# Performance work log

Measured on AMD Instinct MI355X. Metric: run time of the kernel, lower is better.

## Reference

```python
import jax, jax.numpy as jnp
import numpy as np
from jax import lax

C = 256; A = 3; FH = 160; FW = 160
IMG_H = 640.0; IMG_W = 640.0; STRIDE = 4.0; ANCHOR_SIZE = 64.0
OBJ_THR = 0.5; IOU_THR = 0.7; PRE_NMS = 2000; TOP_K = 1000
BN_EPS = 1e-5; NEG = -1e9


def setup_inputs() -> dict:
    key = jax.random.key(0)
    ks = jax.random.split(key, 4)
    s = 0.02
    return {
        "x": jax.random.normal(ks[0], (1, C, FH, FW), jnp.float32),
        "conv_w": jax.random.normal(ks[1], (C, C, 3, 3), jnp.float32) * s,
        "conv_b": jnp.zeros((C,), jnp.float32),
        "bn_gamma": jnp.ones((C,), jnp.float32),
        "bn_beta": jnp.zeros((C,), jnp.float32),
        "bn_mean": jnp.zeros((C,), jnp.float32),
        "bn_var": jnp.ones((C,), jnp.float32),
        "det_w": jax.random.normal(ks[2], (A, C), jnp.float32) * s,
        "det_b": jnp.zeros((A,), jnp.float32),
        "reg_w": jax.random.normal(ks[3], (4 * A, C), jnp.float32) * s,
        "reg_b": jnp.zeros((4 * A,), jnp.float32),
    }


def _make_anchors():
    ars = jnp.array([0.5, 1.0, 2.0], jnp.float32)
    h = ANCHOR_SIZE * jnp.sqrt(ars)
    w = ANCHOR_SIZE / jnp.sqrt(ars)
    base = jnp.stack([-w / 2, -h / 2, w / 2, h / 2], axis=1)  # (A,4)
    sx = jnp.arange(FW, dtype=jnp.float32) * STRIDE
    sy = jnp.arange(FH, dtype=jnp.float32) * STRIDE
    yy, xx = jnp.meshgrid(sy, sx, indexing='ij')  # (FH,FW)
    shifts = jnp.stack([xx, yy, xx, yy], axis=-1)  # (FH,FW,4)
    anchors = base[:, None, None, :] + shifts[None]  # (A,FH,FW,4), anchor-major like RPNHead formatting
    return anchors.reshape(-1, 4)


def _clip(boxes):
    return jnp.stack([
        jnp.clip(boxes[:, 0], 0.0, IMG_W),
        jnp.clip(boxes[:, 1], 0.0, IMG_H),
        jnp.clip(boxes[:, 2], 0.0, IMG_W),
        jnp.clip(boxes[:, 3], 0.0, IMG_H),
    ], axis=1)


def _apply_deltas(boxes, deltas):
    w = boxes[:, 2] - boxes[:, 0]
    h = boxes[:, 3] - boxes[:, 1]
    cx = boxes[:, 0] + 0.5 * w
    cy = boxes[:, 1] + 0.5 * h
    pcx = deltas[:, 0] * w + cx
    pcy = deltas[:, 1] * h + cy
    pw = w * jnp.exp(deltas[:, 2])
    ph = h * jnp.exp(deltas[:, 3])
    return jnp.stack([pcx - 0.5 * pw, pcy - 0.5 * ph, pcx + 0.5 * pw, pcy + 0.5 * ph], axis=1)


def _iou_matrix(b):
    area = (b[:, 2] - b[:, 0]) * (b[:, 3] - b[:, 1])
    lt = jnp.maximum(b[:, None, :2], b[None, :, :2])
    rb = jnp.minimum(b[:, None, 2:], b[None, :, 2:])
    wh = jnp.clip(rb - lt, 0.0)
    inter = wh[..., 0] * wh[..., 1]
    return inter / (area[:, None] + area[None, :] - inter + 1e-9)


def _forward(x, conv_w, conv_b, bn_gamma, bn_beta, bn_mean, bn_var, det_w, det_b, reg_w, reg_b):
    # shared conv + BN(eval) + ReLU
    y = lax.conv_general_dilated(x, conv_w, (1, 1), 'SAME',
                                 dimension_numbers=('NCHW', 'OIHW', 'NCHW')) + conv_b[None, :, None, None]
    scale = bn_gamma / jnp.sqrt(bn_var + BN_EPS)
    y = (y - bn_mean[None, :, None, None]) * scale[None, :, None, None] + bn_beta[None, :, None, None]
    y = jax.nn.relu(y)
    # 1x1 RPN heads
    logits = jnp.einsum('nchw,oc->nohw', y, det_w) + det_b[None, :, None, None]  # (1,A,FH,FW)
    reg = jnp.einsum('nchw,oc->nohw', y, reg_w) + reg_b[None, :, None, None]     # (1,4A,FH,FW)
    # format per RPNHead: (N,1,A,H,W)->permute->(N,A*H*W) and (N,4,A,H,W)->(N,A*H*W,4)
    obj = logits.reshape(1, 1, A, FH, FW).transpose(0, 2, 3, 4, 1).reshape(-1)   # (A*FH*FW,)
    deltas = reg.reshape(1, 4, A, FH, FW).transpose(0, 2, 3, 4, 1).reshape(-1, 4)
    anchors = _clip(_make_anchors())
    proposals = _apply_deltas(anchors, lax.stop_gradient(deltas))
    # _filter_proposals (batch=1)
    lg = lax.stop_gradient(obj)
    props = _clip(proposals)
    score = jax.nn.sigmoid(lg)
    masked = jnp.where(score > OBJ_THR, lg, NEG)  # threshold mask (step 2)
    top_scores, idx = lax.top_k(masked, PRE_NMS)  # pre-NMS top-k (step 3)
    top_boxes = props[idx]
    valid = top_scores > NEG / 2
    iou = _iou_matrix(top_boxes)
    arange = jnp.arange(PRE_NMS)

    def body(i, keep):
        sup = (iou[i] > IOU_THR) & (arange > i)
        return jnp.where(keep[i], keep & ~sup, keep)

    keep = lax.fori_loop(0, PRE_NMS, body, valid)  # greedy NMS (boxes pre-sorted by score)
    rank = jnp.cumsum(keep) - 1
    sel = keep & (rank < TOP_K)
    slot = jnp.where(sel, rank, TOP_K)  # overflow bucket at TOP_K
    filt_logits = jnp.full((TOP_K + 1,), NEG, jnp.float32).at[slot].set(top_scores)[:TOP_K]
    filt_boxes = jnp.zeros((TOP_K + 1, 4), jnp.float32).at[slot].set(top_boxes)[:TOP_K]
    return (anchors, obj, deltas, filt_logits, filt_boxes)


def reference(x, conv_w, conv_b, bn_gamma, bn_beta, bn_mean, bn_var, det_w, det_b, reg_w, reg_b):
    return _forward(x, conv_w, conv_b, bn_gamma, bn_beta, bn_mean, bn_var, det_w, det_b, reg_w, reg_b)
```

## Files before the change

kernel.cpp:

```cpp
#include <hip/hip_runtime.h>
#include <math.h>

#define NPIX  25600
#define NANCH 76800

constexpr int OUT_ANCH = 0;
constexpr int OUT_OBJ  = 307200;
constexpr int OUT_DELT = 384000;
constexpr int OUT_FL   = 691200;
constexpr int OUT_FB   = 692200;

constexpr size_t Y_OFF      = 0;
constexpr size_t PROPS_OFF  = 26214400;
constexpr size_t KEYF_OFF   = PROPS_OFF + 2457600;
constexpr size_t CANDK_OFF  = KEYF_OFF + 307200;
constexpr size_t CANDI_OFF  = CANDK_OFF + 16384;
constexpr size_t TSC_OFF    = CANDI_OFF + 16384;
constexpr size_t TBOX_OFF   = TSC_OFF + 8192;
constexpr size_t HIST_OFF   = TBOX_OFF + 65536;
constexpr size_t STATE_OFF  = HIST_OFF + 1024;
constexpr size_t MASK32_OFF = STATE_OFF + 256;

struct SelState { unsigned prefix; int remaining; int cntHi; int cntEq; };

__device__ __forceinline__ unsigned orderKey32(float f) {
  unsigned u = __float_as_uint(f);
  return (u & 0x80000000u) ? ~u : (u | 0x80000000u);
}
__device__ __forceinline__ float key32ToFloat(unsigned k) {
  unsigned u = (k & 0x80000000u) ? (k & 0x7fffffffu) : ~k;
  return __uint_as_float(u);
}

__global__ __launch_bounds__(256) void init_misc(float* __restrict__ out,
                                                 unsigned* __restrict__ hist,
                                                 SelState* __restrict__ st) {
  int t = blockIdx.x * 256 + threadIdx.x;
  if (t < 1000) out[OUT_FL + t] = -1e9f;
  if (t < 4000) out[OUT_FB + t] = 0.f;
  if (t < 256) hist[t] = 0u;
  if (t == 0) { st->prefix = 0u; st->remaining = 2000; st->cntHi = 0; st->cntEq = 0; }
}

__global__ __launch_bounds__(256) void prep_wt(const float* __restrict__ w,
                                               float* __restrict__ wt) {
  int gid = blockIdx.x * 256 + threadIdx.x;
  int oc  = gid / 2304;
  int rem = gid - oc * 2304;
  int ci  = rem / 9;
  int t   = rem - ci * 9;
  wt[((size_t)ci * 256 + oc) * 9 + t] = w[gid];
}

__global__ __launch_bounds__(256) void conv_hyb_f32r(
    const float* __restrict__ x, const float* __restrict__ wt,
    const float* __restrict__ bv, const float* __restrict__ gamma,
    const float* __restrict__ beta, const float* __restrict__ mean,
    const float* __restrict__ var, float* __restrict__ y) {
  const int tile = blockIdx.x;
  const int th0 = (tile / 10) * 16;
  const int tw0 = (tile - (tile / 10) * 10) * 16;
  const int ob  = blockIdx.y * 32;
  const int tid = threadIdx.x;
  const int wid  = __builtin_amdgcn_readfirstlane(tid >> 6);
  const int lane = tid & 63;
  const int r  = lane >> 2;
  const int cg = lane & 3;
  const int oc0 = ob + wid * 8;

  __shared__ __align__(16) float lin[8][18][20];

  float sreg[11];
  auto loadRegs = [&](int cb) {
#pragma unroll
    for (int k = 0; k < 11; ++k) {
      int idx = tid + k * 256;
      float v = 0.f;
      if (idx < 2592) {
        int ci = idx / 324; int rem = idx - ci * 324;
        int rr = rem / 18;  int cc = rem - rr * 18;
        int gh = th0 + rr - 1, gw = tw0 + cc - 1;
        if ((unsigned)gh < 160u && (unsigned)gw < 160u)
          v = x[(size_t)(cb + ci) * NPIX + gh * 160 + gw];
      }
      sreg[k] = v;
    }
  };
  auto writeRegs = [&]() {
#pragma unroll
    for (int k = 0; k < 11; ++k) {
      int idx = tid + k * 256;
      if (idx < 2592) {
        int ci = idx / 324; int rem = idx - ci * 324;
        int rr = rem / 18;  int cc = rem - rr * 18;
        lin[ci][rr][cc] = sreg[k];
      }
    }
  };

  float acc[8][4];
#pragma unroll
  for (int o = 0; o < 8; ++o)
#pragma unroll
    for (int j = 0; j < 4; ++j) acc[o][j] = 0.f;

  loadRegs(248);
  for (int cb = 248; cb >= 0; cb -= 8) {
    __syncthreads();
    writeRegs();
    __syncthreads();
    if (cb > 0) loadRegs(cb - 8);
#pragma unroll
    for (int ci = 7; ci >= 0; --ci) {
      float in0[6], in1[6], in2[6];
      const float* base = &lin[ci][r][cg * 4];
      {
        float4 q = *(const float4*)(base);
        float2 p = *(const float2*)(base + 4);
        in0[0] = q.x; in0[1] = q.y; in0[2] = q.z; in0[3] = q.w; in0[4] = p.x; in0[5] = p.y;
      }
      {
        float4 q = *(const float4*)(base + 20);
        float2 p = *(const float2*)(base + 24);
        in1[0] = q.x; in1[1] = q.y; in1[2] = q.z; in1[3] = q.w; in1[4] = p.x; in1[5] = p.y;
      }
      {
        float4 q = *(const float4*)(base + 40);
        float2 p = *(const float2*)(base + 44);
        in2[0] = q.x; in2[1] = q.y; in2[2] = q.z; in2[3] = q.w; in2[4] = p.x; in2[5] = p.y;
      }
      const float* wb = wt + ((size_t)(cb + ci) * 256 + oc0) * 9;
#pragma unroll
      for (int o = 0; o < 8; ++o) {
        const float w0 = wb[o * 9 + 0], w1 = wb[o * 9 + 1], w2 = wb[o * 9 + 2];
        const float w3 = wb[o * 9 + 3], w4 = wb[o * 9 + 4], w5 = wb[o * 9 + 5];
        const float w6 = wb[o * 9 + 6], w7 = wb[o * 9 + 7], w8 = wb[o * 9 + 8];
#pragma unroll
        for (int j = 0; j < 4; ++j) {
          float a = acc[o][j];
          a = fmaf(in2[j + 2], w8, a); a = fmaf(in2[j + 1], w7, a); a = fmaf(in2[j + 0], w6, a);
          a = fmaf(in1[j + 2], w5, a); a = fmaf(in1[j + 1], w4, a); a = fmaf(in1[j + 0], w3, a);
          a = fmaf(in0[j + 2], w2, a); a = fmaf(in0[j + 1], w1, a); a = fmaf(in0[j + 0], w0, a);
          acc[o][j] = a;
        }
      }
    }
  }

  const int gh = th0 + r, gw0 = tw0 + cg * 4;
#pragma unroll
  for (int o = 0; o < 8; ++o) {
    int oc = oc0 + o;
    float sc = gamma[oc] / sqrtf(var[oc] + 1e-5f);
    float sh = (bv[oc] - mean[oc]) * sc + beta[oc];
    float4 vv;
    float v0 = fmaf(acc[o][0], sc, sh); vv.x = (v0 > 0.f) ? v0 : 0.f;
    float v1 = fmaf(acc[o][1], sc, sh); vv.y = (v1 > 0.f) ? v1 : 0.f;
    float v2 = fmaf(acc[o][2], sc, sh); vv.z = (v2 > 0.f) ? v2 : 0.f;
    float v3 = fmaf(acc[o][3], sc, sh); vv.w = (v3 > 0.f) ? v3 : 0.f;
    *(float4*)&y[(size_t)oc * NPIX + gh * 160 + gw0] = vv;
  }
}

__global__ __launch_bounds__(256) void heads_kernel(
    const float* __restrict__ y,
    const float* __restrict__ det_w, const float* __restrict__ det_b,
    const float* __restrict__ reg_w, const float* __restrict__ reg_b,
    float* __restrict__ out, double* __restrict__ props,
    float* __restrict__ keyf) {
  const int p = blockIdx.x * 256 + threadIdx.x;
  float od0 = 0.f, od1 = 0.f, od2 = 0.f;
  float rg[12];
#pragma unroll
  for (int o = 0; o < 12; ++o) rg[o] = 0.f;
  const float* yp = y + p;
  for (int c = 255; c >= 0; --c) {
    float v = yp[(size_t)c * NPIX];
    od0 = fmaf(v, det_w[c], od0);
    od1 = fmaf(v, det_w[256 + c], od1);
    od2 = fmaf(v, det_w[512 + c], od2);
#pragma unroll
    for (int o = 0; o < 12; ++o) rg[o] = fmaf(v, reg_w[o * 256 + c], rg[o]);
  }
  const int hh = p / 160;
  const int ww = p - hh * 160;
  const float sx = ww * 4.0f, sy = hh * 4.0f;
  float odv[3] = {od0, od1, od2};
#pragma unroll
  for (int a = 0; a < 3; ++a) {
    float ar = (a == 0) ? 0.5f : ((a == 1) ? 1.0f : 2.0f);
    float sq = sqrtf(ar);
    float haf = 64.0f * sq, waf = 64.0f / sq;
    float ax1 = fminf(fmaxf(sx - waf * 0.5f, 0.f), 640.f);
    float ay1 = fminf(fmaxf(sy - haf * 0.5f, 0.f), 640.f);
    float ax2 = fminf(fmaxf(sx + waf * 0.5f, 0.f), 640.f);
    float ay2 = fminf(fmaxf(sy + haf * 0.5f, 0.f), 640.f);
    int ai = a * NPIX + p;
    out[OUT_ANCH + ai * 4 + 0] = ax1;
    out[OUT_ANCH + ai * 4 + 1] = ay1;
    out[OUT_ANCH + ai * 4 + 2] = ax2;
    out[OUT_ANCH + ai * 4 + 3] = ay2;
    float logit = odv[a] + det_b[a];
    out[OUT_OBJ + ai] = logit;
    float dx = rg[0 + a] + reg_b[0 + a];
    float dy = rg[3 + a] + reg_b[3 + a];
    float dw = rg[6 + a] + reg_b[6 + a];
    float dh = rg[9 + a] + reg_b[9 + a];
    out[OUT_DELT + ai * 4 + 0] = dx;
    out[OUT_DELT + ai * 4 + 1] = dy;
    out[OUT_DELT + ai * 4 + 2] = dw;
    out[OUT_DELT + ai * 4 + 3] = dh;
    float aw = ax2 - ax1, ah = ay2 - ay1;
    float cx = ax1 + 0.5f * aw, cy = ay1 + 0.5f * ah;
    float pcx = dx * aw + cx, pcy = dy * ah + cy;
    float pw = aw * expf(dw), ph = ah * expf(dh);
    props[ai * 4 + 0] = (double)fminf(fmaxf(pcx - 0.5f * pw, 0.f), 640.f);
    props[ai * 4 + 1] = (double)fminf(fmaxf(pcy - 0.5f * ph, 0.f), 640.f);
    props[ai * 4 + 2] = (double)fminf(fmaxf(pcx + 0.5f * pw, 0.f), 640.f);
    props[ai * 4 + 3] = (double)fminf(fmaxf(pcy + 0.5f * ph, 0.f), 640.f);
    keyf[ai] = (logit > 0.f) ? logit : -1e9f;
  }
}

__global__ __launch_bounds__(256) void hist_pass(const float* __restrict__ keyf,
                                                 unsigned* __restrict__ hist,
                                                 const SelState* __restrict__ st, int pass) {
  __shared__ unsigned lh[256];
  lh[threadIdx.x] = 0u;
  __syncthreads();
  unsigned prefix = st->prefix;
  int shift = 24 - 8 * pass;
  int i = blockIdx.x * 256 + threadIdx.x;
  unsigned k = orderKey32(keyf[i]);
  bool ok = (pass == 0) || ((k >> (shift + 8)) == prefix);
  if (ok) atomicAdd(&lh[(k >> shift) & 255u], 1u);
  __syncthreads();
  unsigned c = lh[threadIdx.x];
  if (c) atomicAdd(&hist[threadIdx.x], c);
}

__global__ void pick_kernel(unsigned* __restrict__ hist, SelState* __restrict__ st) {
  if (threadIdx.x == 0 && blockIdx.x == 0) {
    int rem = st->remaining;
    unsigned cum = 0;
    int b = 0;
    for (int i = 255; i >= 0; --i) {
      unsigned h = hist[i];
      if (cum + h >= (unsigned)rem) { b = i; break; }
      cum += h;
    }
    st->prefix = (st->prefix << 8) | (unsigned)b;
    st->remaining = rem - (int)cum;
    for (int i = 0; i < 256; ++i) hist[i] = 0u;
  }
}

__global__ __launch_bounds__(256) void compact_kernel(const float* __restrict__ keyf,
                                                      SelState* __restrict__ st,
                                                      unsigned* __restrict__ candk,
                                                      unsigned* __restrict__ candi) {
  int i = blockIdx.x * 256 + threadIdx.x;
  if (i >= NANCH) return;
  unsigned k = orderKey32(keyf[i]);
  unsigned T = st->prefix;
  if (k > T) {
    int pos = atomicAdd(&st->cntHi, 1);
    if (pos < 2048) { candk[pos] = k; candi[pos] = (unsigned)i; }
  } else if (k == T) {
    int pos = atomicAdd(&st->cntEq, 1);
    if (pos < 2048) { candk[2048 + pos] = k; candi[2048 + pos] = (unsigned)i; }
  }
}

__global__ __launch_bounds__(1024) void sort_gather(const unsigned* __restrict__ candk,
                                                    const unsigned* __restrict__ candi,
                                                    const SelState* __restrict__ st,
                                                    const double* __restrict__ props,
                                                    float* __restrict__ tsc,
                                                    double* __restrict__ tbox) {
  __shared__ unsigned ka[4096];
  __shared__ unsigned ia[4096];
  int nHi = st->cntHi; if (nHi > 2048) nHi = 2048;
  int nEq = st->cntEq; if (nEq > 2048) nEq = 2048;
  for (int i = threadIdx.x; i < 4096; i += 1024) {
    bool real = (i < nHi) || (i >= 2048 && i < 2048 + nEq);
    ka[i] = real ? candk[i] : 0u;
    ia[i] = real ? candi[i] : 0xffffffffu;
  }
  __syncthreads();
  for (int k = 2; k <= 4096; k <<= 1) {
    for (int j = k >> 1; j > 0; j >>= 1) {
      for (int e = threadIdx.x; e < 4096; e += 1024) {
        int l = e ^ j;
        if (l > e) {
          unsigned ke = ka[e], kl = ka[l];
          unsigned ie = ia[e], il = ia[l];
          bool descending = ((e & k) == 0);
          bool lBetter = (kl > ke) || (kl == ke && il < ie);
          bool eBetter = (ke > kl) || (ke == kl && ie < il);
          bool sw = descending ? lBetter : eBetter;
          if (sw) { ka[e] = kl; ka[l] = ke; ia[e] = il; ia[l] = ie; }
        }
      }
      __syncthreads();
    }
  }
  for (int t = threadIdx.x; t < 2000; t += 1024) {
    unsigned idx = ia[t];
    if (idx < (unsigned)NANCH) {
      tsc[t] = key32ToFloat(ka[t]);
      tbox[t * 4 + 0] = props[(size_t)idx * 4 + 0];
      tbox[t * 4 + 1] = props[(size_t)idx * 4 + 1];
      tbox[t * 4 + 2] = props[(size_t)idx * 4 + 2];
      tbox[t * 4 + 3] = props[(size_t)idx * 4 + 3];
    } else {
      tsc[t] = -1e9f;
      tbox[t * 4 + 0] = 0.0; tbox[t * 4 + 1] = 0.0;
      tbox[t * 4 + 2] = 0.0; tbox[t * 4 + 3] = 0.0;
    }
  }
}

__global__ __launch_bounds__(256) void iou_mask(const double* __restrict__ tbox,
                                                unsigned* __restrict__ mask32) {
  int gid = blockIdx.x * 256 + threadIdx.x;
  if (gid >= 2000 * 64) return;
  int i = gid >> 6, l = gid & 63;
  int j0 = l * 32;
  unsigned m = 0u;
  if (j0 + 31 > i) {
    double bix = tbox[i * 4 + 0], biy = tbox[i * 4 + 1];
    double biz = tbox[i * 4 + 2], biw = tbox[i * 4 + 3];
    double areai = (biz - bix) * (biw - biy);
#pragma unroll 4
    for (int b = 0; b < 32; ++b) {
      int j = j0 + b;
      if (j >= 2000 || j <= i) continue;
      double bjx = tbox[j * 4 + 0], bjy = tbox[j * 4 + 1];
      double bjz = tbox[j * 4 + 2], bjw = tbox[j * 4 + 3];
      double xx1 = fmax(bix, bjx), yy1 = fmax(biy, bjy);
      double xx2 = fmin(biz, bjz), yy2 = fmin(biw, bjw);
      double iw = fmax(xx2 - xx1, 0.0), ih = fmax(yy2 - yy1, 0.0);
      double inter = iw * ih;
      double areaj = (bjz - bjx) * (bjw - bjy);
      double iou = inter / (areai + areaj - inter + 1e-9);
      if (iou > 0.7) m |= (1u << b);
    }
  }
  mask32[(size_t)i * 64 + l] = m;
}

__global__ __launch_bounds__(64) void nms_scan(const unsigned* __restrict__ mask32,
                                               const float* __restrict__ tsc,
                                               const double* __restrict__ tbox,
                                               float* __restrict__ out) {
  __shared__ unsigned kw[64];
  __shared__ unsigned wpfx[65];
  __shared__ __align__(16) unsigned stage[2][2048];
  const int lane = threadIdx.x;

  kw[lane] = 0u;
  for (int i = lane; i < 2000; i += 64)
    if (tsc[i] > -5e8f) atomicOr(&kw[i >> 5], 1u << (i & 31));
  const unsigned Vw = kw[lane];
  unsigned S = 0u;

  uint4 s0, s1, s2, s3, s4, s5, s6, s7;
  int nchunks = 0;
  auto stageLoad = [&](int w) {
    int rows = 2000 - w * 32; if (rows > 32) rows = 32;
    nchunks = rows >> 2;
    const uint4* src = (const uint4*)(mask32 + (size_t)w * 2048);
    if (nchunks > 0) s0 = src[0 * 64 + lane];
    if (nchunks > 1) s1 = src[1 * 64 + lane];
    if (nchunks > 2) s2 = src[2 * 64 + lane];
    if (nchunks > 3) s3 = src[3 * 64 + lane];
    if (nchunks > 4) s4 = src[4 * 64 + lane];
    if (nchunks > 5) s5 = src[5 * 64 + lane];
    if (nchunks > 6) s6 = src[6 * 64 + lane];
    if (nchunks > 7) s7 = src[7 * 64 + lane];
  };
  auto stageWrite = [&](int buf) {
    uint4* dst = (uint4*)&stage[buf][0];
    if (nchunks > 0) dst[0 * 64 + lane] = s0;
    if (nchunks > 1) dst[1 * 64 + lane] = s1;
    if (nchunks > 2) dst[2 * 64 + lane] = s2;
    if (nchunks > 3) dst[3 * 64 + lane] = s3;
    if (nchunks > 4) dst[4 * 64 + lane] = s4;
    if (nchunks > 5) dst[5 * 64 + lane] = s5;
    if (nchunks > 6) dst[6 * 64 + lane] = s6;
    if (nchunks > 7) dst[7 * 64 + lane] = s7;
  };

  stageLoad(0);
  stageWrite(0);
  for (int w = 0; w < 63; ++w) {
    const int buf = w & 1;
    if (w + 1 < 63) stageLoad(w + 1);
    unsigned rem = (unsigned)__shfl((int)(Vw & ~S), w);
    while (rem) {
      int b = __ffs(rem) - 1;
      rem &= rem - 1;
      unsigned mlane = stage[buf][b * 64 + lane];
      unsigned supw  = stage[buf][b * 64 + w];
      S |= mlane;
      rem &= ~supw;
    }
    if (w + 1 < 63) stageWrite(buf ^ 1);
  }
  kw[lane] = Vw & ~S;

  if (lane == 0) {
    wpfx[0] = 0;
    for (int w = 0; w < 64; ++w) wpfx[w + 1] = wpfx[w] + __popc(kw[w]);
  }
  for (int i = lane; i < 2000; i += 64) {
    if ((kw[i >> 5] >> (i & 31)) & 1u) {
      int r = (int)wpfx[i >> 5] + __popc(kw[i >> 5] & ((1u << (i & 31)) - 1u));
      if (r < 1000) {
        out[OUT_FL + r] = tsc[i];
        out[OUT_FB + r * 4 + 0] = (float)tbox[i * 4 + 0];
        out[OUT_FB + r * 4 + 1] = (float)tbox[i * 4 + 1];
        out[OUT_FB + r * 4 + 2] = (float)tbox[i * 4 + 2];
        out[OUT_FB + r * 4 + 3] = (float)tbox[i * 4 + 3];
      }
    }
  }
}

extern "C" void kernel_launch(void* const* d_in, const int* in_sizes, int n_in,
                              void* d_out, int out_size, void* d_ws, size_t ws_size,
                              hipStream_t stream) {
  (void)in_sizes; (void)n_in; (void)out_size; (void)ws_size;
  const float* x      = (const float*)d_in[0];
  const float* conv_w = (const float*)d_in[1];
  const float* conv_b = (const float*)d_in[2];
  const float* gamma  = (const float*)d_in[3];
  const float* beta   = (const float*)d_in[4];
  const float* mean   = (const float*)d_in[5];
  const float* var    = (const float*)d_in[6];
  const float* det_w  = (const float*)d_in[7];
  const float* det_b  = (const float*)d_in[8];
  const float* reg_w  = (const float*)d_in[9];
  const float* reg_b  = (const float*)d_in[10];
  float* out = (float*)d_out;
  char* ws = (char*)d_ws;

  float*  y      = (float*)(ws + Y_OFF);
  double* props  = (double*)(ws + PROPS_OFF);
  float*  wt     = (float*)(ws + PROPS_OFF);
  float*  keyf   = (float*)(ws + KEYF_OFF);
  unsigned* candk = (unsigned*)(ws + CANDK_OFF);
  unsigned* candi = (unsigned*)(ws + CANDI_OFF);
  float*  tsc    = (float*)(ws + TSC_OFF);
  double* tbox   = (double*)(ws + TBOX_OFF);
  unsigned* hist = (unsigned*)(ws + HIST_OFF);
  SelState* st   = (SelState*)(ws + STATE_OFF);
  unsigned* mask32 = (unsigned*)(ws + MASK32_OFF);

  init_misc<<<16, 256, 0, stream>>>(out, hist, st);
  prep_wt<<<2304, 256, 0, stream>>>(conv_w, wt);
  conv_hyb_f32r<<<dim3(100, 8), 256, 0, stream>>>(x, wt, conv_b, gamma, beta, mean, var, y);
  heads_kernel<<<100, 256, 0, stream>>>(y, det_w, det_b, reg_w, reg_b, out, props, keyf);
  for (int p = 0; p < 4; ++p) {
    hist_pass<<<300, 256, 0, stream>>>(keyf, hist, st, p);
    pick_kernel<<<1, 64, 0, stream>>>(hist, st);
  }
  compact_kernel<<<300, 256, 0, stream>>>(keyf, st, candk, candi);
  sort_gather<<<1, 1024, 0, stream>>>(candk, candi, st, props, tsc, tbox);
  iou_mask<<<500, 256, 0, stream>>>(tbox, mask32);
  nms_scan<<<1, 64, 0, stream>>>(mask32, tsc, tbox, out);
}
```

Measured before the change: 936.7 us.

## Double-buffer conv weights in registers with vectorized float4 loads

Replaces the per-channel scalar weight loads in the 3x3 conv inner loop with float4 loads into two register buffers, prefetching the next input channel's 72 weights while the current one is computed. The input-tile prefetch is moved to after the first two channels. Launch bounds are changed to request two blocks per CU. The aim is to hide global/L2 latency on weight fetches, at the cost of 144 extra VGPRs that may cause spills or lower occupancy.

```diff
diff --git a/kernel.cpp b/kernel.cpp
--- a/kernel.cpp
+++ b/kernel.cpp
@@ -31,6 +31,9 @@
   unsigned u = (k & 0x80000000u) ? (k & 0x7fffffffu) : ~k;
   return __uint_as_float(u);
 }
+__device__ __forceinline__ float f4c(const float4 v, int c) {
+  return c == 0 ? v.x : (c == 1 ? v.y : (c == 2 ? v.z : v.w));
+}
 
 __global__ __launch_bounds__(256) void init_misc(float* __restrict__ out,
                                                  unsigned* __restrict__ hist,
@@ -52,7 +55,39 @@
   wt[((size_t)ci * 256 + oc) * 9 + t] = w[gid];
 }
 
-__global__ __launch_bounds__(256) void conv_hyb_f32r(
+
+#define WLOAD(WBUF, IC) do {                                                      \
+    const float4* p_ = (const float4*)(wt + (size_t)(IC) * 2304 + (size_t)oc0 * 9); \
+    _Pragma("unroll")                                                             \
+    for (int q_ = 0; q_ < 18; ++q_) WBUF[q_] = p_[q_];                            \
+  } while (0)
+
+#define CONV_COMPUTE(CI, WBUF) do {                                               \
+    float in0[6], in1[6], in2[6];                                                 \
+    const float* base_ = &lin[CI][r][cg * 4];                                     \
+    { float4 q_ = *(const float4*)(base_);      float2 t_ = *(const float2*)(base_ + 4);  \
+      in0[0]=q_.x; in0[1]=q_.y; in0[2]=q_.z; in0[3]=q_.w; in0[4]=t_.x; in0[5]=t_.y; }     \
+    { float4 q_ = *(const float4*)(base_ + 20); float2 t_ = *(const float2*)(base_ + 24); \
+      in1[0]=q_.x; in1[1]=q_.y; in1[2]=q_.z; in1[3]=q_.w; in1[4]=t_.x; in1[5]=t_.y; }     \
+    { float4 q_ = *(const float4*)(base_ + 40); float2 t_ = *(const float2*)(base_ + 44); \
+      in2[0]=q_.x; in2[1]=q_.y; in2[2]=q_.z; in2[3]=q_.w; in2[4]=t_.x; in2[5]=t_.y; }     \
+    _Pragma("unroll")                                                             \
+    for (int o = 0; o < 8; ++o) {                                                 \
+      float w_[9];                                                                \
+      _Pragma("unroll")                                                           \
+      for (int t = 0; t < 9; ++t) { int fi = o * 9 + t; w_[t] = f4c(WBUF[fi >> 2], fi & 3); } \
+      _Pragma("unroll")                                                           \
+      for (int j = 0; j < 4; ++j) {                                               \
+        float a = acc[o][j];                                                      \
+        a = fmaf(in2[j + 2], w_[8], a); a = fmaf(in2[j + 1], w_[7], a); a = fmaf(in2[j + 0], w_[6], a); \
+        a = fmaf(in1[j + 2], w_[5], a); a = fmaf(in1[j + 1], w_[4], a); a = fmaf(in1[j + 0], w_[3], a); \
+        a = fmaf(in0[j + 2], w_[2], a); a = fmaf(in0[j + 1], w_[1], a); a = fmaf(in0[j + 0], w_[0], a); \
+        acc[o][j] = a;                                                            \
+      }                                                                           \
+    }                                                                             \
+  } while (0)
+
+__global__ __launch_bounds__(256, 2) void conv_hyb_f32r(
     const float* __restrict__ x, const float* __restrict__ wt,
     const float* __restrict__ bv, const float* __restrict__ gamma,
     const float* __restrict__ beta, const float* __restrict__ mean,
@@ -104,47 +139,23 @@
 #pragma unroll
     for (int j = 0; j < 4; ++j) acc[o][j] = 0.f;
 
+  float4 wA[18], wB[18];
+
+  WLOAD(wA, 255);
   loadRegs(248);
   for (int cb = 248; cb >= 0; cb -= 8) {
     __syncthreads();
     writeRegs();
     __syncthreads();
+    WLOAD(wB, cb + 6); CONV_COMPUTE(7, wA);
+    WLOAD(wA, cb + 5); CONV_COMPUTE(6, wB);
     if (cb > 0) loadRegs(cb - 8);
-#pragma unroll
-    for (int ci = 7; ci >= 0; --ci) {
-      float in0[6], in1[6], in2[6];
-      const float* base = &lin[ci][r][cg * 4];
-      {
-        float4 q = *(const float4*)(base);
-        float2 p = *(const float2*)(base + 4);
-        in0[0] = q.x; in0[1] = q.y; in0[2] = q.z; in0[3] = q.w; in0[4] = p.x; in0[5] = p.y;
-      }
-      {
-        float4 q = *(const float4*)(base + 20);
-        float2 p = *(const float2*)(base + 24);
-        in1[0] = q.x; in1[1] = q.y; in1[2] = q.z; in1[3] = q.w; in1[4] = p.x; in1[5] = p.y;
-      }
-      {
-        float4 q = *(const float4*)(base + 40);
-        float2 p = *(const float2*)(base + 44);
-        in2[0] = q.x; in2[1] = q.y; in2[2] = q.z; in2[3] = q.w; in2[4] = p.x; in2[5] = p.y;
-      }
-      const float* wb = wt + ((size_t)(cb + ci) * 256 + oc0) * 9;
-#pragma unroll
-      for (int o = 0; o < 8; ++o) {
-        const float w0 = wb[o * 9 + 0], w1 = wb[o * 9 + 1], w2 = wb[o * 9 + 2];
-        const float w3 = wb[o * 9 + 3], w4 = wb[o * 9 + 4], w5 = wb[o * 9 + 5];
-        const float w6 = wb[o * 9 + 6], w7 = wb[o * 9 + 7], w8 = wb[o * 9 + 8];
-#pragma unroll
-        for (int j = 0; j < 4; ++j) {
-          float a = acc[o][j];
-          a = fmaf(in2[j + 2], w8, a); a = fmaf(in2[j + 1], w7, a); a = fmaf(in2[j + 0], w6, a);
-          a = fmaf(in1[j + 2], w5, a); a = fmaf(in1[j + 1], w4, a); a = fmaf(in1[j + 0], w3, a);
-          a = fmaf(in0[j + 2], w2, a); a = fmaf(in0[j + 1], w1, a); a = fmaf(in0[j + 0], w0, a);
-          acc[o][j] = a;
-        }
-      }
-    }
+    WLOAD(wB, cb + 4); CONV_COMPUTE(5, wA);
+    WLOAD(wA, cb + 3); CONV_COMPUTE(4, wB);
+    WLOAD(wB, cb + 2); CONV_COMPUTE(3, wA);
+    WLOAD(wA, cb + 1); CONV_COMPUTE(2, wB);
+    WLOAD(wB, cb + 0); CONV_COMPUTE(1, wA);
+    WLOAD(wA, (cb > 0 ? cb - 1 : 0)); CONV_COMPUTE(0, wB);
   }
 
   const int gh = th0 + r, gw0 = tw0 + cg * 4;
```

New measurement: 1.577 ms. 1.68x slower.

## Fuse init into weight prep, repack head weights, widen heads grid, parallelize pick

Applied to the files above, without the earlier changes.

Merges the init kernel into the weight-transpose kernel, which also repacks det/reg weights into a 16-wide interleaved layout so each channel's head weights sit contiguously. The heads kernel now launches 400 blocks of 64 threads instead of 100 of 256 to cover more CUs. pick_kernel becomes a wavefront-parallel suffix scan using shuffles and ballot instead of a serial single-thread loop. The packed weights reuse the mask32 workspace region, which is only safe because the NMS mask is written later in the stream.

```diff
diff --git a/kernel.cpp b/kernel.cpp
--- a/kernel.cpp
+++ b/kernel.cpp
@@ -32,24 +32,31 @@
   return __uint_as_float(u);
 }
 
-__global__ __launch_bounds__(256) void init_misc(float* __restrict__ out,
-                                                 unsigned* __restrict__ hist,
-                                                 SelState* __restrict__ st) {
-  int t = blockIdx.x * 256 + threadIdx.x;
-  if (t < 1000) out[OUT_FL + t] = -1e9f;
-  if (t < 4000) out[OUT_FB + t] = 0.f;
-  if (t < 256) hist[t] = 0u;
-  if (t == 0) { st->prefix = 0u; st->remaining = 2000; st->cntHi = 0; st->cntEq = 0; }
-}
-
-__global__ __launch_bounds__(256) void prep_wt(const float* __restrict__ w,
-                                               float* __restrict__ wt) {
+__global__ __launch_bounds__(256) void prep_all(const float* __restrict__ w,
+                                                float* __restrict__ wt,
+                                                const float* __restrict__ det_w,
+                                                const float* __restrict__ reg_w,
+                                                float* __restrict__ wt2,
+                                                float* __restrict__ out,
+                                                unsigned* __restrict__ hist,
+                                                SelState* __restrict__ st) {
   int gid = blockIdx.x * 256 + threadIdx.x;
   int oc  = gid / 2304;
   int rem = gid - oc * 2304;
   int ci  = rem / 9;
   int t   = rem - ci * 9;
   wt[((size_t)ci * 256 + oc) * 9 + t] = w[gid];
+  if (gid < 4096) {
+    int c = gid >> 4, j = gid & 15;
+    float v = 0.f;
+    if (j < 3) v = det_w[j * 256 + c];
+    else if (j < 15) v = reg_w[(j - 3) * 256 + c];
+    wt2[gid] = v;
+  }
+  if (gid < 1000) out[OUT_FL + gid] = -1e9f;
+  if (gid < 4000) out[OUT_FB + gid] = 0.f;
+  if (gid < 256) hist[gid] = 0u;
+  if (gid == 0) { st->prefix = 0u; st->remaining = 2000; st->cntHi = 0; st->cntEq = 0; }
 }
 
 __global__ __launch_bounds__(256) void conv_hyb_f32r(
@@ -162,13 +169,12 @@
   }
 }
 
-__global__ __launch_bounds__(256) void heads_kernel(
-    const float* __restrict__ y,
-    const float* __restrict__ det_w, const float* __restrict__ det_b,
-    const float* __restrict__ reg_w, const float* __restrict__ reg_b,
+__global__ __launch_bounds__(64) void heads_kernel(
+    const float* __restrict__ y, const float* __restrict__ wt2,
+    const float* __restrict__ det_b, const float* __restrict__ reg_b,
     float* __restrict__ out, double* __restrict__ props,
     float* __restrict__ keyf) {
-  const int p = blockIdx.x * 256 + threadIdx.x;
+  const int p = blockIdx.x * 64 + threadIdx.x;
   float od0 = 0.f, od1 = 0.f, od2 = 0.f;
   float rg[12];
 #pragma unroll
@@ -176,11 +182,12 @@
   const float* yp = y + p;
   for (int c = 255; c >= 0; --c) {
     float v = yp[(size_t)c * NPIX];
-    od0 = fmaf(v, det_w[c], od0);
-    od1 = fmaf(v, det_w[256 + c], od1);
-    od2 = fmaf(v, det_w[512 + c], od2);
-#pragma unroll
-    for (int o = 0; o < 12; ++o) rg[o] = fmaf(v, reg_w[o * 256 + c], rg[o]);
+    const float* wc = wt2 + c * 16;
+    od0 = fmaf(v, wc[0], od0);
+    od1 = fmaf(v, wc[1], od1);
+    od2 = fmaf(v, wc[2], od2);
+#pragma unroll
+    for (int o = 0; o < 12; ++o) rg[o] = fmaf(v, wc[3 + o], rg[o]);
   }
   const int hh = p / 160;
   const int ww = p - hh * 160;
@@ -239,20 +246,34 @@
   if (c) atomicAdd(&hist[threadIdx.x], c);
 }
 
-__global__ void pick_kernel(unsigned* __restrict__ hist, SelState* __restrict__ st) {
-  if (threadIdx.x == 0 && blockIdx.x == 0) {
-    int rem = st->remaining;
-    unsigned cum = 0;
-    int b = 0;
-    for (int i = 255; i >= 0; --i) {
-      unsigned h = hist[i];
-      if (cum + h >= (unsigned)rem) { b = i; break; }
-      cum += h;
-    }
+__global__ __launch_bounds__(64) void pick_kernel(unsigned* __restrict__ hist,
+                                                  SelState* __restrict__ st) {
+  const int lane = threadIdx.x;
+  const int rem = st->remaining;
+  unsigned h0 = hist[lane * 4 + 0], h1 = hist[lane * 4 + 1];
+  unsigned h2 = hist[lane * 4 + 2], h3 = hist[lane * 4 + 3];
+  unsigned lsum = h0 + h1 + h2 + h3;
+  unsigned acc = lsum;
+#pragma unroll
+  for (int off = 1; off < 64; off <<= 1) {
+    unsigned other = (unsigned)__shfl_down((int)acc, off);
+    if (lane + off < 64) acc += other;
+  }
+  unsigned long long m = __ballot(acc >= (unsigned)rem);
+  int L = 63 - __clzll(m);
+  if (lane == L) {
+    unsigned tail = acc - lsum;
+    unsigned s3 = h3 + tail, s2 = h2 + s3, s1 = h1 + s2, s0 = h0 + s1;
+    int b; unsigned suf, hsel;
+    if (s3 >= (unsigned)rem)      { b = lane * 4 + 3; suf = s3; hsel = h3; }
+    else if (s2 >= (unsigned)rem) { b = lane * 4 + 2; suf = s2; hsel = h2; }
+    else if (s1 >= (unsigned)rem) { b = lane * 4 + 1; suf = s1; hsel = h1; }
+    else                          { b = lane * 4 + 0; suf = s0; hsel = h0; }
     st->prefix = (st->prefix << 8) | (unsigned)b;
-    st->remaining = rem - (int)cum;
-    for (int i = 0; i < 256; ++i) hist[i] = 0u;
-  }
+    st->remaining = rem - (int)(suf - hsel);
+  }
+  hist[lane * 4 + 0] = 0u; hist[lane * 4 + 1] = 0u;
+  hist[lane * 4 + 2] = 0u; hist[lane * 4 + 3] = 0u;
 }
 
 __global__ __launch_bounds__(256) void compact_kernel(const float* __restrict__ keyf,
@@ -457,11 +478,11 @@
   unsigned* hist = (unsigned*)(ws + HIST_OFF);
   SelState* st   = (SelState*)(ws + STATE_OFF);
   unsigned* mask32 = (unsigned*)(ws + MASK32_OFF);
-
-  init_misc<<<16, 256, 0, stream>>>(out, hist, st);
-  prep_wt<<<2304, 256, 0, stream>>>(conv_w, wt);
+  float*  wt2    = (float*)(ws + MASK32_OFF);
+
+  prep_all<<<2304, 256, 0, stream>>>(conv_w, wt, det_w, reg_w, wt2, out, hist, st);
   conv_hyb_f32r<<<dim3(100, 8), 256, 0, stream>>>(x, wt, conv_b, gamma, beta, mean, var, y);
-  heads_kernel<<<100, 256, 0, stream>>>(y, det_w, det_b, reg_w, reg_b, out, props, keyf);
+  heads_kernel<<<400, 64, 0, stream>>>(y, wt2, det_b, reg_b, out, props, keyf);
   for (int p = 0; p < 4; ++p) {
     hist_pass<<<300, 256, 0, stream>>>(keyf, hist, st, p);
     pick_kernel<<<1, 64, 0, stream>>>(hist, st);
```

After: 913.7 us, median of 2. 1.03x faster.
